# Optimization experiments

Measured on AMD Instinct MI355X. Metric: run time of the kernel, lower is better.

## Reference

```python
import jax, jax.numpy as jnp
import numpy as np

NEG = -1e6  # SequenceMask fill value from original code


def setup_inputs() -> dict:
    key = jax.random.key(0)
    ks = jax.random.split(key, 7)
    B, Tq, Tk, U = 32, 1024, 1024, 256
    return {
        "query": jax.random.normal(ks[0], (B, Tq, U), dtype=jnp.float32),
        "key": jax.random.normal(ks[1], (B, Tk, U), dtype=jnp.float32),
        "value": jax.random.normal(ks[2], (B, Tk, U), dtype=jnp.float32),
        "valid_length": jax.random.randint(ks[3], (B,), 0, Tk, dtype=jnp.int32),
        "W_k": jax.random.normal(ks[4], (U, U), dtype=jnp.float32) * (1.0 / np.sqrt(U)),
        "W_q": jax.random.normal(ks[5], (U, U), dtype=jnp.float32) * (1.0 / np.sqrt(U)),
        "v": jax.random.normal(ks[6], (U,), dtype=jnp.float32) * (1.0 / np.sqrt(U)),
    }


def reference(query, key, value, valid_length, W_k, W_q, v):
    # Original applies W_k to query and W_q to key (naming swap kept faithfully).
    tq = jnp.tanh(jnp.einsum('bqu,vu->bqv', query, W_k))  # (B,Tq,U)
    tk = jnp.tanh(jnp.einsum('bku,vu->bkv', key, W_q))    # (B,Tk,U)
    # v is linear over (tq_i + tk_j): decompose to avoid (B,Tq,Tk,U) tensor.
    sq = jnp.einsum('bqu,u->bq', tq, v)  # (B,Tq)
    sk = jnp.einsum('bku,u->bk', tk, v)  # (B,Tk)
    scores = sq[:, :, None] + sk[:, None, :]  # (B,Tq,Tk)
    Tk_ = key.shape[1]
    mask = jnp.arange(Tk_)[None, None, :] < valid_length[:, None, None]  # (B,1,Tk)
    scores = jnp.where(mask, scores, NEG)
    attn = jax.nn.softmax(scores, axis=-1)  # dropout p=0 (eval) -> identity
    return jnp.einsum('bqk,bkd->bqd', attn, value)
```

## Files before the change

### kernel.cpp

```cpp
#include <hip/hip_runtime.h>
#include <hip/hip_fp16.h>
#include <math.h>

#define NB 32
#define TQ 1024
#define TK 1024
#define UD 256

typedef __attribute__((ext_vector_type(8))) _Float16 f16x8;
typedef __attribute__((ext_vector_type(4))) _Float16 f16x4;
typedef __attribute__((ext_vector_type(4))) float f32x4;

__device__ __forceinline__ float fast_tanh(float x) {
  const float e = __expf(2.0f * x);
  return 1.0f - 2.0f / (e + 1.0f);
}

__global__ __launch_bounds__(256) void cvt_wq_kernel(
    const float* __restrict__ Wq, _Float16* __restrict__ wq16t) {
  const int idx = blockIdx.x * 256 + threadIdx.x;
  const int u = idx >> 5;
  const int ks = idx & 31;
  const float4 w0 = *reinterpret_cast<const float4*>(Wq + u * UD + ks * 8);
  const float4 w1 = *reinterpret_cast<const float4*>(Wq + u * UD + ks * 8 + 4);
  f16x8 h;
  h[0] = (_Float16)w0.x; h[1] = (_Float16)w0.y;
  h[2] = (_Float16)w0.z; h[3] = (_Float16)w0.w;
  h[4] = (_Float16)w1.x; h[5] = (_Float16)w1.y;
  h[6] = (_Float16)w1.z; h[7] = (_Float16)w1.w;
  *reinterpret_cast<f16x8*>(wq16t + ((size_t)ks * 256 + u) * 8) = h;
}

__global__ __launch_bounds__(512, 4) void sk_mfma_kernel(
    const float* __restrict__ key, const _Float16* __restrict__ wq16t,
    const float* __restrict__ v, float* __restrict__ sk) {
  __shared__ _Float16 At[32 * 64 * 8];
  __shared__ _Float16 Bt[2][4 * 256 * 8];

  const int tid = threadIdx.x;
  const int lane = tid & 63;
  const int wid = tid >> 6;
  const int wr = wid >> 2;
  const int wc = wid & 3;
  const int lx = lane & 15;
  const int lg = lane >> 4;
  const int row0 = blockIdx.x * 64;

  {
    const int ks = lane >> 1;
    const int jh = lane & 1;
#pragma unroll
    for (int i = 0; i < 8; ++i) {
      const int r = wid * 8 + i;
      const float4 a = *reinterpret_cast<const float4*>(
          key + (size_t)(row0 + r) * UD + lane * 4);
      f16x4 h;
      h[0] = (_Float16)a.x; h[1] = (_Float16)a.y;
      h[2] = (_Float16)a.z; h[3] = (_Float16)a.w;
      const int rs = r ^ (ks & 7);
      *reinterpret_cast<f16x4*>(At + ((ks * 64 + rs) * 8 + jh * 4)) = h;
    }
  }

#pragma unroll
  for (int it = 0; it < 2; ++it) {
    const int f = tid + it * 512;
    *(reinterpret_cast<f16x8*>(Bt[0]) + f) =
        *(reinterpret_cast<const f16x8*>(wq16t) + f);
  }
  __syncthreads();

  f32x4 acc[2][4];
#pragma unroll
  for (int m = 0; m < 2; ++m)
#pragma unroll
    for (int n = 0; n < 4; ++n) acc[m][n] = (f32x4){0.f, 0.f, 0.f, 0.f};

#pragma unroll
  for (int p = 0; p < 8; ++p) {
    const int cur = p & 1;
    if (p < 7) {
#pragma unroll
      for (int it = 0; it < 2; ++it) {
        const int f = tid + it * 512;
        *(reinterpret_cast<f16x8*>(Bt[cur ^ 1]) + f) =
            *(reinterpret_cast<const f16x8*>(wq16t + (size_t)(p + 1) * 8192) +
              f);
      }
    }
    const int ksg = p * 4 + lg;
    f16x8 af[2], bf[4];
#pragma unroll
    for (int m = 0; m < 2; ++m) {
      const int row = wr * 32 + m * 16 + lx;
      const int rs = row ^ (ksg & 7);
      af[m] = *reinterpret_cast<const f16x8*>(At + (ksg * 64 + rs) * 8);
    }
#pragma unroll
    for (int n = 0; n < 4; ++n) {
      const int u = wc * 64 + n * 16 + lx;
      bf[n] = *reinterpret_cast<const f16x8*>(Bt[cur] + (lg * 256 + u) * 8);
    }
#pragma unroll
    for (int m = 0; m < 2; ++m)
#pragma unroll
      for (int n = 0; n < 4; ++n)
        acc[m][n] = __builtin_amdgcn_mfma_f32_16x16x32_f16(af[m], bf[n],
                                                           acc[m][n], 0, 0, 0);
    __syncthreads();
  }

  float vv[4];
#pragma unroll
  for (int n = 0; n < 4; ++n) vv[n] = v[wc * 64 + n * 16 + lx];

  float* red = (float*)At;
  float part[2][4];
#pragma unroll
  for (int m = 0; m < 2; ++m)
#pragma unroll
    for (int r = 0; r < 4; ++r) part[m][r] = 0.f;
#pragma unroll
  for (int m = 0; m < 2; ++m)
#pragma unroll
    for (int n = 0; n < 4; ++n)
#pragma unroll
      for (int r = 0; r < 4; ++r)
        part[m][r] += vv[n] * fast_tanh(acc[m][n][r]);

#pragma unroll
  for (int m = 0; m < 2; ++m)
#pragma unroll
    for (int r = 0; r < 4; ++r) {
      float s = part[m][r];
      s += __shfl_xor(s, 1);
      s += __shfl_xor(s, 2);
      s += __shfl_xor(s, 4);
      s += __shfl_xor(s, 8);
      if (lx == 0) red[(wr * 32 + m * 16 + lg * 4 + r) * 4 + wc] = s;
    }
  __syncthreads();
  if (tid < 64) {
    sk[row0 + tid] = red[tid * 4 + 0] + red[tid * 4 + 1] + red[tid * 4 + 2] +
                     red[tid * 4 + 3];
  }
}

__global__ __launch_bounds__(256) void pv_kernel(
    const float* __restrict__ sk, const int* __restrict__ vlen,
    const float* __restrict__ value, float* __restrict__ part) {
  const int b = blockIdx.x >> 4;
  const int ch = blockIdx.x & 15;
  const int tid = threadIdx.x;
  const int vl = vlen[b];
  __shared__ float wbuf[64];
  __shared__ float red4[8];
  const float* skb = sk + b * TK;

  if (vl == 0) {
    if (tid < 64) wbuf[tid] = 1.0f / (float)TK;
  } else {
    float m = -1e30f;
#pragma unroll
    for (int idx = 0; idx < 4; ++idx) {
      const int k = tid + idx * 256;
      if (k < vl) m = fmaxf(m, skb[k]);
    }
    for (int off = 1; off < 64; off <<= 1) m = fmaxf(m, __shfl_xor(m, off));
    if ((tid & 63) == 0) red4[tid >> 6] = m;
    __syncthreads();
    m = fmaxf(fmaxf(red4[0], red4[1]), fmaxf(red4[2], red4[3]));
    float zs = 0.f;
#pragma unroll
    for (int idx = 0; idx < 4; ++idx) {
      const int k = tid + idx * 256;
      zs += (k < vl) ? __expf(skb[k] - m) : 0.f;
    }
    for (int off = 1; off < 64; off <<= 1) zs += __shfl_xor(zs, off);
    if ((tid & 63) == 0) red4[4 + (tid >> 6)] = zs;
    __syncthreads();
    const float rz = 1.0f / (red4[4] + red4[5] + red4[6] + red4[7]);
    if (tid < 64) {
      const int k = ch * 64 + tid;
      wbuf[tid] = (k < vl) ? __expf(skb[k] - m) * rz : 0.f;
    }
  }
  __syncthreads();

  const int d = tid;
  const float* vb = value + ((size_t)b * TK + ch * 64) * UD;
  float acc = 0.f;
#pragma unroll 8
  for (int k = 0; k < 64; ++k)
    acc = fmaf(wbuf[k], vb[(size_t)k * UD + d], acc);
  part[(size_t)(b * 16 + ch) * UD + d] = acc;
}

__global__ __launch_bounds__(256) void bcast_kernel(
    const float* __restrict__ part, float* __restrict__ out) {
  const int b = blockIdx.x >> 4;
  const int qc = blockIdx.x & 15;
  const int tid = threadIdx.x;
  const int qoff = tid >> 6;
  const int dd = (tid & 63) * 4;

  float4 s = make_float4(0.f, 0.f, 0.f, 0.f);
#pragma unroll
  for (int c = 0; c < 16; ++c) {
    const float4 p = *reinterpret_cast<const float4*>(
        &part[(size_t)(b * 16 + c) * UD + dd]);
    s.x += p.x; s.y += p.y; s.z += p.z; s.w += p.w;
  }

  float* ob = out + (size_t)b * TQ * UD + (size_t)qc * 64 * UD;
#pragma unroll 4
  for (int q4 = 0; q4 < 16; ++q4) {
    *reinterpret_cast<float4*>(&ob[(size_t)(q4 * 4 + qoff) * UD + dd]) = s;
  }
}

extern "C" void kernel_launch(void* const* d_in, const int* in_sizes, int n_in,
                              void* d_out, int out_size, void* d_ws,
                              size_t ws_size, hipStream_t stream) {
  const float* key = (const float*)d_in[1];
  const float* value = (const float*)d_in[2];
  const int* vlen = (const int*)d_in[3];
  const float* Wq = (const float*)d_in[5];
  const float* v = (const float*)d_in[6];
  float* out = (float*)d_out;

  char* ws = (char*)d_ws;
  _Float16* wq16t = (_Float16*)(ws);
  float* sk = (float*)(ws + 131072);
  float* part = (float*)(ws + 262144);

  cvt_wq_kernel<<<32, 256, 0, stream>>>(Wq, wq16t);
  sk_mfma_kernel<<<(NB * TK) / 64, 512, 0, stream>>>(key, wq16t, v, sk);
  pv_kernel<<<NB * 16, 256, 0, stream>>>(sk, vlen, value, part);
  bcast_kernel<<<NB * 16, 256, 0, stream>>>(part, out);
}
```

Baseline: 49.90 us.

## Stream key and weight tiles into LDS via direct global-to-LDS loads, halve row tile

The sk projection kernel now uses global_load_lds to move key rows (kept as fp32) and fp16 weight tiles straight into shared memory, bypassing registers. The key-to-fp16 conversion moves to after the LDS read. The row tile per block shrinks from 64 to 32, so the grid doubles and each wave does one M tile instead of two. The occupancy hint is also dropped. This aims to cut register staging and improve load latency hiding, at the cost of more blocks, more redundant weight streaming per row, and larger fp32 LDS reads.

```diff
diff --git a/kernel.cpp b/kernel.cpp
--- a/kernel.cpp
+++ b/kernel.cpp
@@ -8,12 +8,17 @@
 #define UD 256
 
 typedef __attribute__((ext_vector_type(8))) _Float16 f16x8;
-typedef __attribute__((ext_vector_type(4))) _Float16 f16x4;
 typedef __attribute__((ext_vector_type(4))) float f32x4;
 
 __device__ __forceinline__ float fast_tanh(float x) {
   const float e = __expf(2.0f * x);
   return 1.0f - 2.0f / (e + 1.0f);
+}
+
+__device__ __forceinline__ void gload_lds16(const void* g, void* l) {
+  __builtin_amdgcn_global_load_lds(
+      (const __attribute__((address_space(1))) void*)g,
+      (__attribute__((address_space(3))) void*)l, 16, 0, 0);
 }
 
 __global__ __launch_bounds__(256) void cvt_wq_kernel(
@@ -31,11 +36,11 @@
   *reinterpret_cast<f16x8*>(wq16t + ((size_t)ks * 256 + u) * 8) = h;
 }
 
-__global__ __launch_bounds__(512, 4) void sk_mfma_kernel(
+__global__ __launch_bounds__(512) void sk_mfma_kernel(
     const float* __restrict__ key, const _Float16* __restrict__ wq16t,
     const float* __restrict__ v, float* __restrict__ sk) {
-  __shared__ _Float16 At[32 * 64 * 8];
-  __shared__ _Float16 Bt[2][4 * 256 * 8];
+  __shared__ __align__(16) float At[8192];
+  __shared__ __align__(16) _Float16 Bt[2][8192];
 
   const int tid = threadIdx.x;
   const int lane = tid & 63;
@@ -44,69 +49,60 @@
   const int wc = wid & 3;
   const int lx = lane & 15;
   const int lg = lane >> 4;
-  const int row0 = blockIdx.x * 64;
-
-  {
-    const int ks = lane >> 1;
-    const int jh = lane & 1;
-#pragma unroll
-    for (int i = 0; i < 8; ++i) {
-      const int r = wid * 8 + i;
-      const float4 a = *reinterpret_cast<const float4*>(
-          key + (size_t)(row0 + r) * UD + lane * 4);
-      f16x4 h;
-      h[0] = (_Float16)a.x; h[1] = (_Float16)a.y;
-      h[2] = (_Float16)a.z; h[3] = (_Float16)a.w;
-      const int rs = r ^ (ks & 7);
-      *reinterpret_cast<f16x4*>(At + ((ks * 64 + rs) * 8 + jh * 4)) = h;
-    }
-  }
-
-#pragma unroll
-  for (int it = 0; it < 2; ++it) {
-    const int f = tid + it * 512;
-    *(reinterpret_cast<f16x8*>(Bt[0]) + f) =
-        *(reinterpret_cast<const f16x8*>(wq16t) + f);
+  const int row0 = blockIdx.x * 32;
+
+#pragma unroll
+  for (int i = 0; i < 4; ++i) {
+    const int ks = i * 8 + wid;
+    const int slot_log = lane ^ (ks & 7);
+    const int r = slot_log >> 1;
+    const int h = slot_log & 1;
+    gload_lds16(key + (size_t)(row0 + r) * UD + ks * 8 + h * 4,
+                (char*)At + ks * 1024);
+  }
+#pragma unroll
+  for (int i = 0; i < 2; ++i) {
+    const int Sw = i * 512 + wid * 64;
+    gload_lds16(wq16t + (size_t)(Sw + lane) * 8, (char*)Bt[0] + Sw * 16);
   }
   __syncthreads();
 
-  f32x4 acc[2][4];
-#pragma unroll
-  for (int m = 0; m < 2; ++m)
-#pragma unroll
-    for (int n = 0; n < 4; ++n) acc[m][n] = (f32x4){0.f, 0.f, 0.f, 0.f};
+  f32x4 acc[4];
+#pragma unroll
+  for (int n = 0; n < 4; ++n) acc[n] = (f32x4){0.f, 0.f, 0.f, 0.f};
 
 #pragma unroll
   for (int p = 0; p < 8; ++p) {
     const int cur = p & 1;
     if (p < 7) {
 #pragma unroll
-      for (int it = 0; it < 2; ++it) {
-        const int f = tid + it * 512;
-        *(reinterpret_cast<f16x8*>(Bt[cur ^ 1]) + f) =
-            *(reinterpret_cast<const f16x8*>(wq16t + (size_t)(p + 1) * 8192) +
-              f);
+      for (int i = 0; i < 2; ++i) {
+        const int Sw = i * 512 + wid * 64;
+        gload_lds16(wq16t + (size_t)(p + 1) * 8192 + (size_t)(Sw + lane) * 8,
+                    (char*)Bt[cur ^ 1] + Sw * 16);
       }
     }
     const int ksg = p * 4 + lg;
-    f16x8 af[2], bf[4];
-#pragma unroll
-    for (int m = 0; m < 2; ++m) {
-      const int row = wr * 32 + m * 16 + lx;
-      const int rs = row ^ (ksg & 7);
-      af[m] = *reinterpret_cast<const f16x8*>(At + (ksg * 64 + rs) * 8);
-    }
-#pragma unroll
-    for (int n = 0; n < 4; ++n) {
-      const int u = wc * 64 + n * 16 + lx;
-      bf[n] = *reinterpret_cast<const f16x8*>(Bt[cur] + (lg * 256 + u) * 8);
-    }
-#pragma unroll
-    for (int m = 0; m < 2; ++m)
-#pragma unroll
-      for (int n = 0; n < 4; ++n)
-        acc[m][n] = __builtin_amdgcn_mfma_f32_16x16x32_f16(af[m], bf[n],
-                                                           acc[m][n], 0, 0, 0);
+    const int row = wr * 16 + lx;
+    const float* ap0 =
+        At + ksg * 256 + ((row * 2) ^ (ksg & 7)) * 4;
+    const float* ap1 =
+        At + ksg * 256 + ((row * 2 + 1) ^ (ksg & 7)) * 4;
+    const f32x4 alo = *reinterpret_cast<const f32x4*>(ap0);
+    const f32x4 ahi = *reinterpret_cast<const f32x4*>(ap1);
+    f16x8 af;
+    af[0] = (_Float16)alo[0]; af[1] = (_Float16)alo[1];
+    af[2] = (_Float16)alo[2]; af[3] = (_Float16)alo[3];
+    af[4] = (_Float16)ahi[0]; af[5] = (_Float16)ahi[1];
+    af[6] = (_Float16)ahi[2]; af[7] = (_Float16)ahi[3];
+    f16x8 bf[4];
+#pragma unroll
+    for (int n = 0; n < 4; ++n)
+      bf[n] = *reinterpret_cast<const f16x8*>(
+          Bt[cur] + ((size_t)(lg * 256 + wc * 64 + n * 16 + lx)) * 8);
+#pragma unroll
+    for (int n = 0; n < 4; ++n)
+      acc[n] = __builtin_amdgcn_mfma_f32_16x16x32_f16(af, bf[n], acc[n], 0, 0, 0);
     __syncthreads();
   }
 
@@ -115,32 +111,23 @@
   for (int n = 0; n < 4; ++n) vv[n] = v[wc * 64 + n * 16 + lx];
 
   float* red = (float*)At;
-  float part[2][4];
-#pragma unroll
-  for (int m = 0; m < 2; ++m)
-#pragma unroll
-    for (int r = 0; r < 4; ++r) part[m][r] = 0.f;
-#pragma unroll
-  for (int m = 0; m < 2; ++m)
-#pragma unroll
-    for (int n = 0; n < 4; ++n)
-#pragma unroll
-      for (int r = 0; r < 4; ++r)
-        part[m][r] += vv[n] * fast_tanh(acc[m][n][r]);
-
-#pragma unroll
-  for (int m = 0; m < 2; ++m)
-#pragma unroll
-    for (int r = 0; r < 4; ++r) {
-      float s = part[m][r];
-      s += __shfl_xor(s, 1);
-      s += __shfl_xor(s, 2);
-      s += __shfl_xor(s, 4);
-      s += __shfl_xor(s, 8);
-      if (lx == 0) red[(wr * 32 + m * 16 + lg * 4 + r) * 4 + wc] = s;
-    }
+  float part[4] = {0.f, 0.f, 0.f, 0.f};
+#pragma unroll
+  for (int n = 0; n < 4; ++n)
+#pragma unroll
+    for (int r = 0; r < 4; ++r) part[r] += vv[n] * fast_tanh(acc[n][r]);
+
+#pragma unroll
+  for (int r = 0; r < 4; ++r) {
+    float s = part[r];
+    s += __shfl_xor(s, 1);
+    s += __shfl_xor(s, 2);
+    s += __shfl_xor(s, 4);
+    s += __shfl_xor(s, 8);
+    if (lx == 0) red[(wr * 16 + lg * 4 + r) * 4 + wc] = s;
+  }
   __syncthreads();
-  if (tid < 64) {
+  if (tid < 32) {
     sk[row0 + tid] = red[tid * 4 + 0] + red[tid * 4 + 1] + red[tid * 4 + 2] +
                      red[tid * 4 + 3];
   }
@@ -235,7 +222,7 @@
   float* part = (float*)(ws + 262144);
 
   cvt_wq_kernel<<<32, 256, 0, stream>>>(Wq, wq16t);
-  sk_mfma_kernel<<<(NB * TK) / 64, 512, 0, stream>>>(key, wq16t, v, sk);
+  sk_mfma_kernel<<<(NB * TK) / 32, 512, 0, stream>>>(key, wq16t, v, sk);
   pv_kernel<<<NB * 16, 256, 0, stream>>>(sk, vlen, value, part);
   bcast_kernel<<<NB * 16, 256, 0, stream>>>(part, out);
 }
```

New measurement: 51.88 us. 1.04x slower.

## Shrink sk MFMA tile to 32 rows and read W_q fragments from global

Applied to the files above, without the earlier changes.

The key-projection kernel now uses 256-thread blocks over 32 key rows instead of 512 threads over 64 rows. It no longer double-buffers the converted W_q through shared memory. Each wave loads its B fragments straight from global memory (cached in L2), which drops the per-step barriers and most of the LDS footprint. The trade-off is that each block re-reads the full W_q from cache, and twice as many blocks are launched.

```diff
diff --git a/kernel.cpp b/kernel.cpp
--- a/kernel.cpp
+++ b/kernel.cpp
@@ -31,44 +31,38 @@
   *reinterpret_cast<f16x8*>(wq16t + ((size_t)ks * 256 + u) * 8) = h;
 }
 
-__global__ __launch_bounds__(512, 4) void sk_mfma_kernel(
+__global__ __launch_bounds__(256, 4) void sk_mfma_kernel(
     const float* __restrict__ key, const _Float16* __restrict__ wq16t,
     const float* __restrict__ v, float* __restrict__ sk) {
-  __shared__ _Float16 At[32 * 64 * 8];
-  __shared__ _Float16 Bt[2][4 * 256 * 8];
+  __shared__ _Float16 As[32 * 32 * 8];
 
   const int tid = threadIdx.x;
   const int lane = tid & 63;
-  const int wid = tid >> 6;
-  const int wr = wid >> 2;
-  const int wc = wid & 3;
+  const int wc = tid >> 6;
   const int lx = lane & 15;
   const int lg = lane >> 4;
-  const int row0 = blockIdx.x * 64;
+  const int row0 = blockIdx.x * 32;
 
   {
     const int ks = lane >> 1;
     const int jh = lane & 1;
 #pragma unroll
     for (int i = 0; i < 8; ++i) {
-      const int r = wid * 8 + i;
+      const int r = wc * 8 + i;
       const float4 a = *reinterpret_cast<const float4*>(
           key + (size_t)(row0 + r) * UD + lane * 4);
       f16x4 h;
       h[0] = (_Float16)a.x; h[1] = (_Float16)a.y;
       h[2] = (_Float16)a.z; h[3] = (_Float16)a.w;
-      const int rs = r ^ (ks & 7);
-      *reinterpret_cast<f16x4*>(At + ((ks * 64 + rs) * 8 + jh * 4)) = h;
-    }
-  }
-
-#pragma unroll
-  for (int it = 0; it < 2; ++it) {
-    const int f = tid + it * 512;
-    *(reinterpret_cast<f16x8*>(Bt[0]) + f) =
-        *(reinterpret_cast<const f16x8*>(wq16t) + f);
-  }
-  __syncthreads();
+      const int rs = r ^ ((ks & 3) << 2);
+      *reinterpret_cast<f16x4*>(As + ((ks * 32 + rs) * 8 + jh * 4)) = h;
+    }
+  }
+  __syncthreads();
+
+  float vv[4];
+#pragma unroll
+  for (int n = 0; n < 4; ++n) vv[n] = v[wc * 64 + n * 16 + lx];
 
   f32x4 acc[2][4];
 #pragma unroll
@@ -77,44 +71,35 @@
     for (int n = 0; n < 4; ++n) acc[m][n] = (f32x4){0.f, 0.f, 0.f, 0.f};
 
 #pragma unroll
-  for (int p = 0; p < 8; ++p) {
-    const int cur = p & 1;
-    if (p < 7) {
-#pragma unroll
-      for (int it = 0; it < 2; ++it) {
-        const int f = tid + it * 512;
-        *(reinterpret_cast<f16x8*>(Bt[cur ^ 1]) + f) =
-            *(reinterpret_cast<const f16x8*>(wq16t + (size_t)(p + 1) * 8192) +
-              f);
+  for (int q = 0; q < 4; ++q) {
+    f16x8 bf[2][4];
+#pragma unroll
+    for (int kq = 0; kq < 2; ++kq)
+#pragma unroll
+      for (int n = 0; n < 4; ++n) {
+        const int ks = q * 8 + kq * 4 + lg;
+        bf[kq][n] = *reinterpret_cast<const f16x8*>(
+            wq16t + ((size_t)ks * 256 + wc * 64 + n * 16 + lx) * 8);
       }
-    }
-    const int ksg = p * 4 + lg;
-    f16x8 af[2], bf[4];
-#pragma unroll
-    for (int m = 0; m < 2; ++m) {
-      const int row = wr * 32 + m * 16 + lx;
-      const int rs = row ^ (ksg & 7);
-      af[m] = *reinterpret_cast<const f16x8*>(At + (ksg * 64 + rs) * 8);
-    }
-#pragma unroll
-    for (int n = 0; n < 4; ++n) {
-      const int u = wc * 64 + n * 16 + lx;
-      bf[n] = *reinterpret_cast<const f16x8*>(Bt[cur] + (lg * 256 + u) * 8);
-    }
-#pragma unroll
-    for (int m = 0; m < 2; ++m)
-#pragma unroll
-      for (int n = 0; n < 4; ++n)
-        acc[m][n] = __builtin_amdgcn_mfma_f32_16x16x32_f16(af[m], bf[n],
-                                                           acc[m][n], 0, 0, 0);
-    __syncthreads();
-  }
-
-  float vv[4];
-#pragma unroll
-  for (int n = 0; n < 4; ++n) vv[n] = v[wc * 64 + n * 16 + lx];
-
-  float* red = (float*)At;
+#pragma unroll
+    for (int kq = 0; kq < 2; ++kq) {
+      const int ks = q * 8 + kq * 4 + lg;
+      f16x8 af[2];
+#pragma unroll
+      for (int m = 0; m < 2; ++m) {
+        const int rs = (m * 16 + lx) ^ ((ks & 3) << 2);
+        af[m] = *reinterpret_cast<const f16x8*>(As + (ks * 32 + rs) * 8);
+      }
+#pragma unroll
+      for (int m = 0; m < 2; ++m)
+#pragma unroll
+        for (int n = 0; n < 4; ++n)
+          acc[m][n] = __builtin_amdgcn_mfma_f32_16x16x32_f16(
+              af[m], bf[kq][n], acc[m][n], 0, 0, 0);
+    }
+  }
+
+  float* red = (float*)As;
   float part[2][4];
 #pragma unroll
   for (int m = 0; m < 2; ++m)
@@ -128,6 +113,7 @@
       for (int r = 0; r < 4; ++r)
         part[m][r] += vv[n] * fast_tanh(acc[m][n][r]);
 
+  __syncthreads();
 #pragma unroll
   for (int m = 0; m < 2; ++m)
 #pragma unroll
@@ -137,10 +123,10 @@
       s += __shfl_xor(s, 2);
       s += __shfl_xor(s, 4);
       s += __shfl_xor(s, 8);
-      if (lx == 0) red[(wr * 32 + m * 16 + lg * 4 + r) * 4 + wc] = s;
-    }
-  __syncthreads();
-  if (tid < 64) {
+      if (lx == 0) red[(m * 16 + lg * 4 + r) * 4 + wc] = s;
+    }
+  __syncthreads();
+  if (tid < 32) {
     sk[row0 + tid] = red[tid * 4 + 0] + red[tid * 4 + 1] + red[tid * 4 + 2] +
                      red[tid * 4 + 3];
   }
@@ -235,7 +221,7 @@
   float* part = (float*)(ws + 262144);
 
   cvt_wq_kernel<<<32, 256, 0, stream>>>(Wq, wq16t);
-  sk_mfma_kernel<<<(NB * TK) / 64, 512, 0, stream>>>(key, wq16t, v, sk);
+  sk_mfma_kernel<<<(NB * TK) / 32, 256, 0, stream>>>(key, wq16t, v, sk);
   pv_kernel<<<NB * 16, 256, 0, stream>>>(sk, vlen, value, part);
   bcast_kernel<<<NB * 16, 256, 0, stream>>>(part, out);
 }
```

Measured after the change: 48.11 us. 1.04x faster.

## Fuse W_q fp16 conversion into sk MFMA kernel with K-chunked staging

Applied to the files above, without the earlier changes.

Removes the separate W_q conversion kernel. Each block of the sk kernel now loads fp32 key and W_q directly and converts them to fp16 inside the kernel, streaming them into shared memory in four K-chunks of 64. This saves one launch and the workspace round trip, and lowers shared memory per block. In exchange, every block re-reads and re-converts the fp32 W_q (256 KB per block, served from cache). The double buffering is gone, so loads no longer overlap the MFMA work, and the XOR swizzle on the A tile is dropped, which may cause LDS bank conflicts.

```diff
diff --git a/kernel.cpp b/kernel.cpp
--- a/kernel.cpp
+++ b/kernel.cpp
@@ -8,7 +8,6 @@
 #define UD 256
 
 typedef __attribute__((ext_vector_type(8))) _Float16 f16x8;
-typedef __attribute__((ext_vector_type(4))) _Float16 f16x4;
 typedef __attribute__((ext_vector_type(4))) float f32x4;
 
 __device__ __forceinline__ float fast_tanh(float x) {
@@ -16,26 +15,20 @@
   return 1.0f - 2.0f / (e + 1.0f);
 }
 
-__global__ __launch_bounds__(256) void cvt_wq_kernel(
-    const float* __restrict__ Wq, _Float16* __restrict__ wq16t) {
-  const int idx = blockIdx.x * 256 + threadIdx.x;
-  const int u = idx >> 5;
-  const int ks = idx & 31;
-  const float4 w0 = *reinterpret_cast<const float4*>(Wq + u * UD + ks * 8);
-  const float4 w1 = *reinterpret_cast<const float4*>(Wq + u * UD + ks * 8 + 4);
+__device__ __forceinline__ f16x8 cvt2(const float4 a, const float4 b) {
   f16x8 h;
-  h[0] = (_Float16)w0.x; h[1] = (_Float16)w0.y;
-  h[2] = (_Float16)w0.z; h[3] = (_Float16)w0.w;
-  h[4] = (_Float16)w1.x; h[5] = (_Float16)w1.y;
-  h[6] = (_Float16)w1.z; h[7] = (_Float16)w1.w;
-  *reinterpret_cast<f16x8*>(wq16t + ((size_t)ks * 256 + u) * 8) = h;
+  h[0] = (_Float16)a.x; h[1] = (_Float16)a.y;
+  h[2] = (_Float16)a.z; h[3] = (_Float16)a.w;
+  h[4] = (_Float16)b.x; h[5] = (_Float16)b.y;
+  h[6] = (_Float16)b.z; h[7] = (_Float16)b.w;
+  return h;
 }
 
 __global__ __launch_bounds__(512, 4) void sk_mfma_kernel(
-    const float* __restrict__ key, const _Float16* __restrict__ wq16t,
+    const float* __restrict__ key, const float* __restrict__ Wq,
     const float* __restrict__ v, float* __restrict__ sk) {
-  __shared__ _Float16 At[32 * 64 * 8];
-  __shared__ _Float16 Bt[2][4 * 256 * 8];
+  __shared__ _Float16 Bt[8 * 256 * 8];
+  __shared__ _Float16 At[8 * 64 * 8];
 
   const int tid = threadIdx.x;
   const int lane = tid & 63;
@@ -46,29 +39,8 @@
   const int lg = lane >> 4;
   const int row0 = blockIdx.x * 64;
 
-  {
-    const int ks = lane >> 1;
-    const int jh = lane & 1;
-#pragma unroll
-    for (int i = 0; i < 8; ++i) {
-      const int r = wid * 8 + i;
-      const float4 a = *reinterpret_cast<const float4*>(
-          key + (size_t)(row0 + r) * UD + lane * 4);
-      f16x4 h;
-      h[0] = (_Float16)a.x; h[1] = (_Float16)a.y;
-      h[2] = (_Float16)a.z; h[3] = (_Float16)a.w;
-      const int rs = r ^ (ks & 7);
-      *reinterpret_cast<f16x4*>(At + ((ks * 64 + rs) * 8 + jh * 4)) = h;
-    }
-  }
-
-#pragma unroll
-  for (int it = 0; it < 2; ++it) {
-    const int f = tid + it * 512;
-    *(reinterpret_cast<f16x8*>(Bt[0]) + f) =
-        *(reinterpret_cast<const f16x8*>(wq16t) + f);
-  }
-  __syncthreads();
+  const int ar = tid & 63, ah = tid >> 6;
+  const int bu = tid & 255, bg = tid >> 8;
 
   f32x4 acc[2][4];
 #pragma unroll
@@ -76,37 +48,45 @@
 #pragma unroll
     for (int n = 0; n < 4; ++n) acc[m][n] = (f32x4){0.f, 0.f, 0.f, 0.f};
 
-#pragma unroll
-  for (int p = 0; p < 8; ++p) {
-    const int cur = p & 1;
-    if (p < 7) {
-#pragma unroll
-      for (int it = 0; it < 2; ++it) {
-        const int f = tid + it * 512;
-        *(reinterpret_cast<f16x8*>(Bt[cur ^ 1]) + f) =
-            *(reinterpret_cast<const f16x8*>(wq16t + (size_t)(p + 1) * 8192) +
-              f);
+  for (int p = 0; p < 4; ++p) {
+    const int k0 = p * 64;
+    {
+      const float* ga = key + (size_t)(row0 + ar) * UD + k0 + ah * 8;
+      const float4 a0 = *reinterpret_cast<const float4*>(ga);
+      const float4 a1 = *reinterpret_cast<const float4*>(ga + 4);
+      *reinterpret_cast<f16x8*>(At + ((ah << 6) + ar) * 8) = cvt2(a0, a1);
+    }
+    {
+      const float* gb = Wq + (size_t)bu * UD + k0 + bg * 32;
+#pragma unroll
+      for (int gg = 0; gg < 4; ++gg) {
+        const float4 b0 = *reinterpret_cast<const float4*>(gb + gg * 8);
+        const float4 b1 = *reinterpret_cast<const float4*>(gb + gg * 8 + 4);
+        const int ks = bg * 4 + gg;
+        *reinterpret_cast<f16x8*>(Bt + ((ks << 8) + bu) * 8) = cvt2(b0, b1);
       }
     }
-    const int ksg = p * 4 + lg;
-    f16x8 af[2], bf[4];
-#pragma unroll
-    for (int m = 0; m < 2; ++m) {
-      const int row = wr * 32 + m * 16 + lx;
-      const int rs = row ^ (ksg & 7);
-      af[m] = *reinterpret_cast<const f16x8*>(At + (ksg * 64 + rs) * 8);
-    }
-#pragma unroll
-    for (int n = 0; n < 4; ++n) {
-      const int u = wc * 64 + n * 16 + lx;
-      bf[n] = *reinterpret_cast<const f16x8*>(Bt[cur] + (lg * 256 + u) * 8);
-    }
-#pragma unroll
-    for (int m = 0; m < 2; ++m)
+    __syncthreads();
+
+#pragma unroll
+    for (int kc = 0; kc < 2; ++kc) {
+      const int ks = kc * 4 + lg;
+      f16x8 af[2], bf[4];
+#pragma unroll
+      for (int m = 0; m < 2; ++m)
+        af[m] = *reinterpret_cast<const f16x8*>(
+            At + ((ks << 6) + wr * 32 + m * 16 + lx) * 8);
 #pragma unroll
       for (int n = 0; n < 4; ++n)
-        acc[m][n] = __builtin_amdgcn_mfma_f32_16x16x32_f16(af[m], bf[n],
-                                                           acc[m][n], 0, 0, 0);
+        bf[n] = *reinterpret_cast<const f16x8*>(
+            Bt + ((ks << 8) + wc * 64 + n * 16 + lx) * 8);
+#pragma unroll
+      for (int m = 0; m < 2; ++m)
+#pragma unroll
+        for (int n = 0; n < 4; ++n)
+          acc[m][n] = __builtin_amdgcn_mfma_f32_16x16x32_f16(
+              af[m], bf[n], acc[m][n], 0, 0, 0);
+    }
     __syncthreads();
   }
 
@@ -230,12 +210,10 @@
   float* out = (float*)d_out;
 
   char* ws = (char*)d_ws;
-  _Float16* wq16t = (_Float16*)(ws);
-  float* sk = (float*)(ws + 131072);
-  float* part = (float*)(ws + 262144);
-
-  cvt_wq_kernel<<<32, 256, 0, stream>>>(Wq, wq16t);
-  sk_mfma_kernel<<<(NB * TK) / 64, 512, 0, stream>>>(key, wq16t, v, sk);
+  float* sk = (float*)(ws);
+  float* part = (float*)(ws + 131072);
+
+  sk_mfma_kernel<<<(NB * TK) / 64, 512, 0, stream>>>(key, Wq, v, sk);
   pv_kernel<<<NB * 16, 256, 0, stream>>>(sk, vlen, value, part);
   bcast_kernel<<<NB * 16, 256, 0, stream>>>(part, out);
 }
```

Measured after the change: 54.85 us. 9.9% more time.
